# Optimization experiments

Hardware: AMD Instinct MI355X
Metric: run time of the kernel (lower is better)

The kernel has to match this reference:

```python
import jax, jax.numpy as jnp
import numpy as np

B, T, C = 32, 128, 64
E, H = 8, 4            # feat_dim, num_heads
D = E // H             # head_dim = 2
HID = 32               # hidden_dim


def setup_inputs() -> dict:
    key = jax.random.key(0)
    ks = jax.random.split(key, 20)
    s = 0.1
    return {
        "x": jax.random.normal(ks[0], (B, T, C), jnp.float32),
        # input_proj: Linear(C, C)
        "W_in": jax.random.normal(ks[1], (C, C), jnp.float32) * s,
        "b_in": jax.random.normal(ks[2], (C,), jnp.float32) * s,
        # time_step_score: Linear(C, C//4) -> GELU -> Linear(C//4, 1) -> Sigmoid
        "W_ts1": jax.random.normal(ks[3], (C // 4, C), jnp.float32) * s,
        "b_ts1": jax.random.normal(ks[4], (C // 4,), jnp.float32) * s,
        "W_ts2": jax.random.normal(ks[5], (1, C // 4), jnp.float32) * s,
        "b_ts2": jax.random.normal(ks[6], (1,), jnp.float32) * s,
        # per-channel GRU(1 -> E): torch gate order (r, z, n)
        "W_ih": jax.random.normal(ks[7], (C, 3 * E), jnp.float32) * s,      # input size 1
        "W_hh": jax.random.normal(ks[8], (C, 3 * E, E), jnp.float32) * s,
        "b_ih": jax.random.normal(ks[9], (C, 3 * E), jnp.float32) * s,
        "b_hh": jax.random.normal(ks[10], (C, 3 * E), jnp.float32) * s,
        # shared MultiheadAttention(E, 4): packed in_proj + out_proj
        "W_qkv": jax.random.normal(ks[11], (3 * E, E), jnp.float32) * s,
        "b_qkv": jax.random.normal(ks[12], (3 * E,), jnp.float32) * s,
        "W_o": jax.random.normal(ks[13], (E, E), jnp.float32) * s,
        "b_o": jax.random.normal(ks[14], (E,), jnp.float32) * s,
        # out_proj: Linear(C*E, HID)
        "W_out": jax.random.normal(ks[15], (HID, C * E), jnp.float32) * s,
        "b_out": jax.random.normal(ks[16], (HID,), jnp.float32) * s,
    }


def _forward(x, W_in, b_in, W_ts1, b_ts1, W_ts2, b_ts2,
             W_ih, W_hh, b_ih, b_hh, W_qkv, b_qkv, W_o, b_o, W_out, b_out):
    bs, ts, c = x.shape
    # time step importance: per-timestep MLP over the raw features
    h1 = jax.nn.gelu(jnp.einsum('btc,fc->btf', x, W_ts1) + b_ts1, approximate=False)
    ts_imp = jax.nn.sigmoid(jnp.einsum('btf,of->bto', h1, W_ts2) + b_ts2)[..., 0]  # [B,T]

    xp = jnp.einsum('btc,dc->btd', x, W_in) + b_in  # [B,T,C]

    # Batched per-channel GRU scan over time. state h: [B,C,E]
    def step(h, x_t):
        gi = x_t[:, :, None] * W_ih[None] + b_ih          # [B,C,3E]
        gh = jnp.einsum('bce,cge->bcg', h, W_hh) + b_hh   # [B,C,3E]
        ir, iz, inn = gi[..., :E], gi[..., E:2 * E], gi[..., 2 * E:]
        hr, hz, hn = gh[..., :E], gh[..., E:2 * E], gh[..., 2 * E:]
        r = jax.nn.sigmoid(ir + hr)
        z = jax.nn.sigmoid(iz + hz)
        n = jnp.tanh(inn + r * hn)
        h_new = (1.0 - z) * n + z * h
        return h_new, h_new

    h0 = jnp.zeros((bs, c, E), xp.dtype)
    _, hs = jax.lax.scan(step, h0, jnp.transpose(xp, (1, 0, 2)))  # [T,B,C,E]
    hs_bcte = jnp.transpose(hs, (1, 2, 0, 3))                     # [B,C,T,E]

    # Shared MHA applied independently per channel (batched over B*C)
    qkv = jnp.einsum('bcte,fe->bctf', hs_bcte, W_qkv) + b_qkv     # [B,C,T,3E]
    q, k, v = qkv[..., :E], qkv[..., E:2 * E], qkv[..., 2 * E:]
    def heads(t):
        return t.reshape(bs, c, ts, H, D)
    q, k, v = heads(q), heads(k), heads(v)
    scores = jnp.einsum('bcthd,bcshd->bchts', q, k) / np.sqrt(D)
    attn = jax.nn.softmax(scores, axis=-1)
    o = jnp.einsum('bchts,bcshd->bcthd', attn, v).reshape(bs, c, ts, E)
    attn_out = jnp.einsum('bcte,fe->bctf', o, W_o) + b_o          # [B,C,T,E]
    attention = jnp.transpose(attn_out, (0, 2, 1, 3))             # [B,T,C,E]

    out_flat = jnp.transpose(hs, (1, 0, 2, 3)).reshape(bs, ts, c * E)  # [B,T,C*E]
    out = jnp.einsum('btf,hf->bth', out_flat, W_out) + b_out           # [B,T,HID]

    feat_imp = jax.nn.sigmoid(attention.sum(axis=(1, 3)))   # [B,C]
    tsf_imp = jax.nn.sigmoid(attention.sum(axis=-1))        # [B,T,C]
    return out[:, -1, :], feat_imp, ts_imp, tsf_imp


def reference(x, W_in, b_in, W_ts1, b_ts1, W_ts2, b_ts2,
              W_ih, W_hh, b_ih, b_hh, W_qkv, b_qkv, W_o, b_o, W_out, b_out):
    return _forward(x, W_in, b_in, W_ts1, b_ts1, W_ts2, b_ts2,
                    W_ih, W_hh, b_ih, b_hh, W_qkv, b_qkv, W_o, b_o, W_out, b_out)
```

## Files before the change

kernel.cpp:

```cpp
#include <hip/hip_runtime.h>
#include <hip/hip_bf16.h>
#include <math.h>

#define B_ 32
#define T_ 128
#define C_ 64
#define E_ 8
#define HID_ 32

#define LOG2E 1.44269504088896341f

__device__ __forceinline__ float fast_rcp(float x) { return __builtin_amdgcn_rcpf(x); }
__device__ __forceinline__ float fast_sigmoid(float x) {
    return fast_rcp(1.0f + exp2f(-LOG2E * x));
}
__device__ __forceinline__ float fast_tanh(float x) {
    float xc = fminf(fmaxf(x, -15.0f), 15.0f);
    float t = exp2f(2.0f * LOG2E * xc);
    return (t - 1.0f) * fast_rcp(t + 1.0f);
}

__global__ __launch_bounds__(64) void k_gru(
    const float* __restrict__ x, const float* __restrict__ W_in, const float* __restrict__ b_in,
    const float* __restrict__ W_ih, const float* __restrict__ W_hh,
    const float* __restrict__ b_ih, const float* __restrict__ b_hh,
    float* __restrict__ hs, float* __restrict__ fh)
{
    const int tid = threadIdx.x;
    const int ci = tid >> 3;
    const int e = tid & 7;
    const int chain = blockIdx.x * 8 + ci;
    const int b = chain >> 6;
    const int c = chain & 63;

    __shared__ float wsh[8][C_];
    __shared__ float xc[8][T_ + 1];

#pragma unroll
    for (int i = 0; i < 8; ++i) {
        int idx = tid * 8 + i;
        int ci2 = idx >> 6;
        int cc = (blockIdx.x * 8 + ci2) & 63;
        wsh[ci2][idx & 63] = W_in[cc * C_ + (idx & 63)];
    }
    __syncthreads();

    const float bi = b_in[c];
    for (int tt = 0; tt < 16; ++tt) {
        const int t = e * 16 + tt;
        const float4* xr = (const float4*)(x + (b * T_ + t) * C_);
        float a = bi;
#pragma unroll
        for (int k4 = 0; k4 < 16; ++k4) {
            float4 xv = xr[k4];
            a = fmaf(xv.x, wsh[ci][k4 * 4 + 0], a);
            a = fmaf(xv.y, wsh[ci][k4 * 4 + 1], a);
            a = fmaf(xv.z, wsh[ci][k4 * 4 + 2], a);
            a = fmaf(xv.w, wsh[ci][k4 * 4 + 3], a);
        }
        xc[ci][t] = a;
    }
    __syncthreads();

    float wr[E_], wz[E_], wn[E_];
#pragma unroll
    for (int j = 0; j < E_; ++j) {
        wr[j] = W_hh[(c * 24 + 0 * E_ + e) * E_ + j];
        wz[j] = W_hh[(c * 24 + 1 * E_ + e) * E_ + j];
        wn[j] = W_hh[(c * 24 + 2 * E_ + e) * E_ + j];
    }
    const float wir = W_ih[c * 24 + e], wiz = W_ih[c * 24 + E_ + e], win = W_ih[c * 24 + 2 * E_ + e];
    const float bir = b_ih[c * 24 + e], biz = b_ih[c * 24 + E_ + e], bin_ = b_ih[c * 24 + 2 * E_ + e];
    const float bhr = b_hh[c * 24 + e], bhz = b_hh[c * 24 + E_ + e], bhn = b_hh[c * 24 + 2 * E_ + e];

    float h = 0.0f;
    float* ho = hs + (size_t)chain * T_ * E_ + e;
    for (int t = 0; t < T_; ++t) {
        float xv = xc[ci][t];
        float gr = fmaf(xv, wir, bir) + bhr;
        float gz = fmaf(xv, wiz, biz) + bhz;
        float gn = fmaf(xv, win, bin_);
        float hn = bhn;
#pragma unroll
        for (int j = 0; j < E_; ++j) {
            float hj = __shfl(h, j, E_);
            gr = fmaf(hj, wr[j], gr);
            gz = fmaf(hj, wz[j], gz);
            hn = fmaf(hj, wn[j], hn);
        }
        float r = fast_sigmoid(gr);
        float z = fast_sigmoid(gz);
        float nn = fast_tanh(fmaf(r, hn, gn));
        h = fmaf(z, h - nn, nn);
        ho[t * E_] = h;
    }
    fh[chain * E_ + e] = h;
}

__global__ __launch_bounds__(128) void k_attn(
    const float* __restrict__ hs, const float* __restrict__ W_qkv, const float* __restrict__ b_qkv,
    const float* __restrict__ W_o, const float* __restrict__ b_o,
    float* __restrict__ feat_imp, float* __restrict__ tsf_imp)
{
    const int bc = blockIdx.x;
    const int b = bc >> 6, c = bc & 63;
    const int tid = threadIdx.x;
    const int r = tid >> 1;
    const int p = tid & 1;

    __shared__ __align__(16) float hsl[T_][E_];
    __shared__ __align__(16) float ks[T_][E_];
    __shared__ __align__(16) float vs[T_][E_];
    __shared__ float wssum[E_];
    __shared__ float bsum_s;
    __shared__ float red[T_];

    {
        const float4* hp = (const float4*)(hs + (size_t)bc * T_ * E_ + tid * E_);
        ((float4*)&hsl[tid][0])[0] = hp[0];
        ((float4*)&hsl[tid][0])[1] = hp[1];
    }
    if (tid < E_) {
        float ws = 0.0f;
#pragma unroll
        for (int fp = 0; fp < E_; ++fp) ws += W_o[fp * E_ + tid];
        wssum[tid] = ws;
    }
    if (tid == E_) {
        float bs = 0.0f;
#pragma unroll
        for (int fp = 0; fp < E_; ++fp) bs += b_o[fp];
        bsum_s = bs;
    }
    __syncthreads();

    const float qscale = 0.70710678118654752f * LOG2E;
    {
        float hr[E_];
#pragma unroll
        for (int j = 0; j < E_; ++j) hr[j] = hsl[tid][j];
#pragma unroll
        for (int f = 0; f < E_; ++f) {
            float a = b_qkv[E_ + f];
#pragma unroll
            for (int j = 0; j < E_; ++j) a = fmaf(hr[j], W_qkv[(E_ + f) * E_ + j], a);
            ks[tid][f] = a;
        }
#pragma unroll
        for (int f = 0; f < E_; ++f) {
            float a = b_qkv[2 * E_ + f];
#pragma unroll
            for (int j = 0; j < E_; ++j) a = fmaf(hr[j], W_qkv[(2 * E_ + f) * E_ + j], a);
            vs[tid][f] = a;
        }
    }
    float q0[E_], q1[E_];
#pragma unroll
    for (int f = 0; f < E_; ++f) {
        float a0 = b_qkv[f], a1 = b_qkv[f];
#pragma unroll
        for (int j = 0; j < E_; ++j) {
            float w = W_qkv[f * E_ + j];
            a0 = fmaf(hsl[r][j], w, a0);
            a1 = fmaf(hsl[r + 64][j], w, a1);
        }
        q0[f] = a0 * qscale;
        q1[f] = a1 * qscale;
    }
    __syncthreads();

    float l0[4] = {0.f,0.f,0.f,0.f}, l1[4] = {0.f,0.f,0.f,0.f};
    float a0[E_] = {0.f,0.f,0.f,0.f,0.f,0.f,0.f,0.f};
    float a1[E_] = {0.f,0.f,0.f,0.f,0.f,0.f,0.f,0.f};
    const float* kb = &ks[p * 64][0];
    const float* vb = &vs[p * 64][0];
#pragma unroll 8
    for (int i = 0; i < 64; ++i) {
        float4 k0 = *(const float4*)(kb + i * 8);
        float4 k1 = *(const float4*)(kb + i * 8 + 4);
        float4 v0 = *(const float4*)(vb + i * 8);
        float4 v1 = *(const float4*)(vb + i * 8 + 4);
        float p00 = exp2f(fmaf(q0[1], k0.y, q0[0] * k0.x));
        float p01 = exp2f(fmaf(q0[3], k0.w, q0[2] * k0.z));
        float p02 = exp2f(fmaf(q0[5], k1.y, q0[4] * k1.x));
        float p03 = exp2f(fmaf(q0[7], k1.w, q0[6] * k1.z));
        float p10 = exp2f(fmaf(q1[1], k0.y, q1[0] * k0.x));
        float p11 = exp2f(fmaf(q1[3], k0.w, q1[2] * k0.z));
        float p12 = exp2f(fmaf(q1[5], k1.y, q1[4] * k1.x));
        float p13 = exp2f(fmaf(q1[7], k1.w, q1[6] * k1.z));
        l0[0] += p00; l0[1] += p01; l0[2] += p02; l0[3] += p03;
        l1[0] += p10; l1[1] += p11; l1[2] += p12; l1[3] += p13;
        a0[0] = fmaf(p00, v0.x, a0[0]); a0[1] = fmaf(p00, v0.y, a0[1]);
        a0[2] = fmaf(p01, v0.z, a0[2]); a0[3] = fmaf(p01, v0.w, a0[3]);
        a0[4] = fmaf(p02, v1.x, a0[4]); a0[5] = fmaf(p02, v1.y, a0[5]);
        a0[6] = fmaf(p03, v1.z, a0[6]); a0[7] = fmaf(p03, v1.w, a0[7]);
        a1[0] = fmaf(p10, v0.x, a1[0]); a1[1] = fmaf(p10, v0.y, a1[1]);
        a1[2] = fmaf(p11, v0.z, a1[2]); a1[3] = fmaf(p11, v0.w, a1[3]);
        a1[4] = fmaf(p12, v1.x, a1[4]); a1[5] = fmaf(p12, v1.y, a1[5]);
        a1[6] = fmaf(p13, v1.z, a1[6]); a1[7] = fmaf(p13, v1.w, a1[7]);
    }

#pragma unroll
    for (int i = 0; i < 4; ++i) {
        l0[i] += __shfl_xor(l0[i], 1);
        l1[i] += __shfl_xor(l1[i], 1);
    }
#pragma unroll
    for (int j = 0; j < E_; ++j) {
        a0[j] += __shfl_xor(a0[j], 1);
        a1[j] += __shfl_xor(a1[j], 1);
    }

    const float* lm = p ? l1 : l0;
    const float* am = p ? a1 : a0;
    const int row = p ? (r + 64) : r;
    float S = bsum_s;
#pragma unroll
    for (int f = 0; f < E_; ++f)
        S = fmaf(am[f] * fast_rcp(lm[f >> 1]), wssum[f], S);

    tsf_imp[(size_t)b * T_ * C_ + (size_t)row * C_ + c] = fast_sigmoid(S);
    red[row] = S;
    __syncthreads();
    for (int off = 64; off > 0; off >>= 1) {
        if (tid < off) red[tid] += red[tid + off];
        __syncthreads();
    }
    if (tid == 0) feat_imp[bc] = fast_sigmoid(red[0]);
}

__global__ __launch_bounds__(64) void k_ts(
    const float* __restrict__ x,
    const float* __restrict__ W_ts1, const float* __restrict__ b_ts1,
    const float* __restrict__ W_ts2, const float* __restrict__ b_ts2,
    float* __restrict__ ts_imp)
{
    const int bt = blockIdx.x;
    const int tid = threadIdx.x;
    __shared__ float xs[C_];
    __shared__ float h1[16];
    xs[tid] = x[bt * C_ + tid];
    __syncthreads();
    if (tid < 16) {
        float a = b_ts1[tid];
#pragma unroll
        for (int k = 0; k < C_; ++k) a = fmaf(xs[k], W_ts1[tid * C_ + k], a);
        h1[tid] = 0.5f * a * (1.0f + erff(a * 0.70710678118654752f));
    }
    __syncthreads();
    if (tid == 0) {
        float s = b_ts2[0];
#pragma unroll
        for (int k = 0; k < 16; ++k) s = fmaf(h1[k], W_ts2[k], s);
        ts_imp[bt] = fast_sigmoid(s);
    }
}

__global__ __launch_bounds__(64) void k_out(
    const float* __restrict__ fh, const float* __restrict__ W_out, const float* __restrict__ b_out,
    float* __restrict__ out0)
{
    const int b = blockIdx.x;
    const int tid = threadIdx.x;
    __shared__ float hf[C_ * E_];
    const float4* src = (const float4*)(fh + (b * C_ + tid) * E_);
    float4* dst = (float4*)(hf + tid * E_);
    dst[0] = src[0];
    dst[1] = src[1];
    __syncthreads();
    if (tid < HID_) {
        float a = b_out[tid];
        const float* wo = W_out + tid * (C_ * E_);
        for (int k = 0; k < C_ * E_; ++k) a = fmaf(hf[k], wo[k], a);
        out0[b * HID_ + tid] = a;
    }
}

extern "C" void kernel_launch(void* const* d_in, const int* in_sizes, int n_in,
                              void* d_out, int out_size, void* d_ws, size_t ws_size,
                              hipStream_t stream) {
    (void)in_sizes; (void)n_in; (void)out_size; (void)ws_size;

    float* out0 = (float*)d_out;
    float* feat = out0 + B_ * HID_;
    float* tsim = feat + B_ * C_;
    float* tsf  = tsim + B_ * T_;

    const float* x     = (const float*)d_in[0];
    const float* W_in  = (const float*)d_in[1];
    const float* b_in  = (const float*)d_in[2];
    const float* W_ts1 = (const float*)d_in[3];
    const float* b_ts1 = (const float*)d_in[4];
    const float* W_ts2 = (const float*)d_in[5];
    const float* b_ts2 = (const float*)d_in[6];
    const float* W_ih  = (const float*)d_in[7];
    const float* W_hh  = (const float*)d_in[8];
    const float* b_ih  = (const float*)d_in[9];
    const float* b_hh  = (const float*)d_in[10];
    const float* W_qkv = (const float*)d_in[11];
    const float* b_qkv = (const float*)d_in[12];
    const float* W_o   = (const float*)d_in[13];
    const float* b_o   = (const float*)d_in[14];
    const float* W_out = (const float*)d_in[15];
    const float* b_out = (const float*)d_in[16];

    float* fhb = (float*)d_ws;
    float* hsb = fhb + B_ * C_ * E_;

    hipLaunchKernelGGL(k_gru, dim3(B_ * C_ / 8), dim3(64), 0, stream,
                       x, W_in, b_in, W_ih, W_hh, b_ih, b_hh, hsb, fhb);
    hipLaunchKernelGGL(k_attn, dim3(B_ * C_), dim3(128), 0, stream,
                       hsb, W_qkv, b_qkv, W_o, b_o, feat, tsf);
    hipLaunchKernelGGL(k_ts, dim3(B_ * T_), dim3(64), 0, stream,
                       x, W_ts1, b_ts1, W_ts2, b_ts2, tsim);
    hipLaunchKernelGGL(k_out, dim3(B_), dim3(64), 0, stream,
                       fhb, W_out, b_out, out0);
}
```

Before: 110.6 us.

## Fold W_o into V, split attention keys across 256 threads, shorten GRU dependency chain

The attention kernel now only computes what the outputs need: the sum over output features. It precomputes per-row dot products of V with the column sums of W_o, so it no longer accumulates the full 8-wide P·V. Keys are split across four 64-thread groups (256 threads per block), and the partial softmax sums are combined through shared memory. In the GRU recurrence, the matvec is rewritten as a tree of pairwise products instead of a serial FMA chain, the r/z biases are pre-added and the next input is prefetched, all to cut per-step latency. This adds extra shared memory and a synchronization step for the partial reduction, and the x prefetch reads one element past the end of each row on the last step.

```diff
diff --git a/kernel.cpp b/kernel.cpp
--- a/kernel.cpp
+++ b/kernel.cpp
@@ -15,7 +15,7 @@
     return fast_rcp(1.0f + exp2f(-LOG2E * x));
 }
 __device__ __forceinline__ float fast_tanh(float x) {
-    float xc = fminf(fmaxf(x, -15.0f), 15.0f);
+    float xc = __builtin_amdgcn_fmed3f(x, -15.0f, 15.0f);
     float t = exp2f(2.0f * LOG2E * xc);
     return (t - 1.0f) * fast_rcp(t + 1.0f);
 }
@@ -70,34 +70,49 @@
         wn[j] = W_hh[(c * 24 + 2 * E_ + e) * E_ + j];
     }
     const float wir = W_ih[c * 24 + e], wiz = W_ih[c * 24 + E_ + e], win = W_ih[c * 24 + 2 * E_ + e];
-    const float bir = b_ih[c * 24 + e], biz = b_ih[c * 24 + E_ + e], bin_ = b_ih[c * 24 + 2 * E_ + e];
-    const float bhr = b_hh[c * 24 + e], bhz = b_hh[c * 24 + E_ + e], bhn = b_hh[c * 24 + 2 * E_ + e];
+    const float cr = b_ih[c * 24 + e] + b_hh[c * 24 + e];
+    const float cz = b_ih[c * 24 + E_ + e] + b_hh[c * 24 + E_ + e];
+    const float bin_ = b_ih[c * 24 + 2 * E_ + e];
+    const float bhn  = b_hh[c * 24 + 2 * E_ + e];
 
     float h = 0.0f;
+    float xv = xc[ci][0];
     float* ho = hs + (size_t)chain * T_ * E_ + e;
     for (int t = 0; t < T_; ++t) {
-        float xv = xc[ci][t];
-        float gr = fmaf(xv, wir, bir) + bhr;
-        float gz = fmaf(xv, wiz, biz) + bhz;
-        float gn = fmaf(xv, win, bin_);
-        float hn = bhn;
-#pragma unroll
-        for (int j = 0; j < E_; ++j) {
-            float hj = __shfl(h, j, E_);
-            gr = fmaf(hj, wr[j], gr);
-            gz = fmaf(hj, wz[j], gz);
-            hn = fmaf(hj, wn[j], hn);
-        }
+        float xvn = xc[ci][t + 1];
+        float hj0 = __shfl(h, 0, 8), hj1 = __shfl(h, 1, 8);
+        float hj2 = __shfl(h, 2, 8), hj3 = __shfl(h, 3, 8);
+        float hj4 = __shfl(h, 4, 8), hj5 = __shfl(h, 5, 8);
+        float hj6 = __shfl(h, 6, 8), hj7 = __shfl(h, 7, 8);
+        float grx = fmaf(xv, wir, cr);
+        float gzx = fmaf(xv, wiz, cz);
+        float gnx = fmaf(xv, win, bin_);
+        float r0 = fmaf(hj1, wr[1], hj0 * wr[0]);
+        float r1 = fmaf(hj3, wr[3], hj2 * wr[2]);
+        float r2 = fmaf(hj5, wr[5], hj4 * wr[4]);
+        float r3 = fmaf(hj7, wr[7], hj6 * wr[6]);
+        float z0 = fmaf(hj1, wz[1], hj0 * wz[0]);
+        float z1 = fmaf(hj3, wz[3], hj2 * wz[2]);
+        float z2 = fmaf(hj5, wz[5], hj4 * wz[4]);
+        float z3 = fmaf(hj7, wz[7], hj6 * wz[6]);
+        float n0 = fmaf(hj1, wn[1], hj0 * wn[0]);
+        float n1 = fmaf(hj3, wn[3], hj2 * wn[2]);
+        float n2 = fmaf(hj5, wn[5], hj4 * wn[4]);
+        float n3 = fmaf(hj7, wn[7], hj6 * wn[6]);
+        float gr = grx + ((r0 + r1) + (r2 + r3));
+        float gz = gzx + ((z0 + z1) + (z2 + z3));
+        float hn = bhn + ((n0 + n1) + (n2 + n3));
         float r = fast_sigmoid(gr);
         float z = fast_sigmoid(gz);
-        float nn = fast_tanh(fmaf(r, hn, gn));
+        float nn = fast_tanh(fmaf(r, hn, gnx));
         h = fmaf(z, h - nn, nn);
         ho[t * E_] = h;
+        xv = xvn;
     }
     fh[chain * E_ + e] = h;
 }
 
-__global__ __launch_bounds__(128) void k_attn(
+__global__ __launch_bounds__(256) void k_attn(
     const float* __restrict__ hs, const float* __restrict__ W_qkv, const float* __restrict__ b_qkv,
     const float* __restrict__ W_o, const float* __restrict__ b_o,
     float* __restrict__ feat_imp, float* __restrict__ tsf_imp)
@@ -105,81 +120,80 @@
     const int bc = blockIdx.x;
     const int b = bc >> 6, c = bc & 63;
     const int tid = threadIdx.x;
-    const int r = tid >> 1;
-    const int p = tid & 1;
-
-    __shared__ __align__(16) float hsl[T_][E_];
+    const int t2 = tid & 63;
+    const int sq = tid >> 6;
+
     __shared__ __align__(16) float ks[T_][E_];
-    __shared__ __align__(16) float vs[T_][E_];
-    __shared__ float wssum[E_];
-    __shared__ float bsum_s;
+    __shared__ __align__(16) float us[T_][4];
+    __shared__ float qsT[E_][T_];
+    __shared__ float pacc[3][T_][8];
     __shared__ float red[T_];
 
+    const float qscale = 0.70710678118654752f * LOG2E;
+
     {
-        const float4* hp = (const float4*)(hs + (size_t)bc * T_ * E_ + tid * E_);
-        ((float4*)&hsl[tid][0])[0] = hp[0];
-        ((float4*)&hsl[tid][0])[1] = hp[1];
-    }
-    if (tid < E_) {
-        float ws = 0.0f;
-#pragma unroll
-        for (int fp = 0; fp < E_; ++fp) ws += W_o[fp * E_ + tid];
-        wssum[tid] = ws;
-    }
-    if (tid == E_) {
-        float bs = 0.0f;
-#pragma unroll
-        for (int fp = 0; fp < E_; ++fp) bs += b_o[fp];
-        bsum_s = bs;
-    }
-    __syncthreads();
-
-    const float qscale = 0.70710678118654752f * LOG2E;
-    {
-        float hr[E_];
-#pragma unroll
-        for (int j = 0; j < E_; ++j) hr[j] = hsl[tid][j];
-#pragma unroll
-        for (int f = 0; f < E_; ++f) {
-            float a = b_qkv[E_ + f];
-#pragma unroll
-            for (int j = 0; j < E_; ++j) a = fmaf(hr[j], W_qkv[(E_ + f) * E_ + j], a);
-            ks[tid][f] = a;
+        const int row = (tid < 128) ? tid : (tid - 128);
+        const float4* hp = (const float4*)(hs + (size_t)bc * T_ * E_ + row * E_);
+        float4 h0 = hp[0], h1 = hp[1];
+        float hr[E_] = {h0.x, h0.y, h0.z, h0.w, h1.x, h1.y, h1.z, h1.w};
+        if (tid < 128) {
+            float kv[E_];
+#pragma unroll
+            for (int f = 0; f < E_; ++f) {
+                float a = b_qkv[E_ + f];
+#pragma unroll
+                for (int j = 0; j < E_; ++j) a = fmaf(hr[j], W_qkv[(E_ + f) * E_ + j], a);
+                kv[f] = a;
+            }
+            ((float4*)&ks[row][0])[0] = make_float4(kv[0], kv[1], kv[2], kv[3]);
+            ((float4*)&ks[row][0])[1] = make_float4(kv[4], kv[5], kv[6], kv[7]);
+#pragma unroll
+            for (int f = 0; f < E_; ++f) {
+                float a = b_qkv[f];
+#pragma unroll
+                for (int j = 0; j < E_; ++j) a = fmaf(hr[j], W_qkv[f * E_ + j], a);
+                qsT[f][row] = a * qscale;
+            }
+        } else {
+            float ws[E_];
+#pragma unroll
+            for (int d = 0; d < E_; ++d) {
+                float w = 0.0f;
+#pragma unroll
+                for (int fp = 0; fp < E_; ++fp) w += W_o[fp * E_ + d];
+                ws[d] = w;
+            }
+            float vv[E_];
+#pragma unroll
+            for (int f = 0; f < E_; ++f) {
+                float a = b_qkv[2 * E_ + f];
+#pragma unroll
+                for (int j = 0; j < E_; ++j) a = fmaf(hr[j], W_qkv[(2 * E_ + f) * E_ + j], a);
+                vv[f] = a;
+            }
+            float4 uu;
+            uu.x = fmaf(vv[1], ws[1], vv[0] * ws[0]);
+            uu.y = fmaf(vv[3], ws[3], vv[2] * ws[2]);
+            uu.z = fmaf(vv[5], ws[5], vv[4] * ws[4]);
+            uu.w = fmaf(vv[7], ws[7], vv[6] * ws[6]);
+            *((float4*)&us[row][0]) = uu;
         }
-#pragma unroll
-        for (int f = 0; f < E_; ++f) {
-            float a = b_qkv[2 * E_ + f];
-#pragma unroll
-            for (int j = 0; j < E_; ++j) a = fmaf(hr[j], W_qkv[(2 * E_ + f) * E_ + j], a);
-            vs[tid][f] = a;
-        }
-    }
+    }
+    __syncthreads();
+
     float q0[E_], q1[E_];
 #pragma unroll
-    for (int f = 0; f < E_; ++f) {
-        float a0 = b_qkv[f], a1 = b_qkv[f];
-#pragma unroll
-        for (int j = 0; j < E_; ++j) {
-            float w = W_qkv[f * E_ + j];
-            a0 = fmaf(hsl[r][j], w, a0);
-            a1 = fmaf(hsl[r + 64][j], w, a1);
-        }
-        q0[f] = a0 * qscale;
-        q1[f] = a1 * qscale;
-    }
-    __syncthreads();
-
-    float l0[4] = {0.f,0.f,0.f,0.f}, l1[4] = {0.f,0.f,0.f,0.f};
-    float a0[E_] = {0.f,0.f,0.f,0.f,0.f,0.f,0.f,0.f};
-    float a1[E_] = {0.f,0.f,0.f,0.f,0.f,0.f,0.f,0.f};
-    const float* kb = &ks[p * 64][0];
-    const float* vb = &vs[p * 64][0];
+    for (int f = 0; f < E_; ++f) { q0[f] = qsT[f][t2]; q1[f] = qsT[f][t2 + 64]; }
+
+    float l0[4] = {0.f,0.f,0.f,0.f}, S0[4] = {0.f,0.f,0.f,0.f};
+    float l1[4] = {0.f,0.f,0.f,0.f}, S1[4] = {0.f,0.f,0.f,0.f};
+    const float* kb = &ks[sq * 32][0];
+    const float* ub = &us[sq * 32][0];
 #pragma unroll 8
-    for (int i = 0; i < 64; ++i) {
+    for (int i = 0; i < 32; ++i) {
         float4 k0 = *(const float4*)(kb + i * 8);
         float4 k1 = *(const float4*)(kb + i * 8 + 4);
-        float4 v0 = *(const float4*)(vb + i * 8);
-        float4 v1 = *(const float4*)(vb + i * 8 + 4);
+        float4 uu = *(const float4*)(ub + i * 4);
         float p00 = exp2f(fmaf(q0[1], k0.y, q0[0] * k0.x));
         float p01 = exp2f(fmaf(q0[3], k0.w, q0[2] * k0.z));
         float p02 = exp2f(fmaf(q0[5], k1.y, q0[4] * k1.x));
@@ -190,37 +204,45 @@
         float p13 = exp2f(fmaf(q1[7], k1.w, q1[6] * k1.z));
         l0[0] += p00; l0[1] += p01; l0[2] += p02; l0[3] += p03;
         l1[0] += p10; l1[1] += p11; l1[2] += p12; l1[3] += p13;
-        a0[0] = fmaf(p00, v0.x, a0[0]); a0[1] = fmaf(p00, v0.y, a0[1]);
-        a0[2] = fmaf(p01, v0.z, a0[2]); a0[3] = fmaf(p01, v0.w, a0[3]);
-        a0[4] = fmaf(p02, v1.x, a0[4]); a0[5] = fmaf(p02, v1.y, a0[5]);
-        a0[6] = fmaf(p03, v1.z, a0[6]); a0[7] = fmaf(p03, v1.w, a0[7]);
-        a1[0] = fmaf(p10, v0.x, a1[0]); a1[1] = fmaf(p10, v0.y, a1[1]);
-        a1[2] = fmaf(p11, v0.z, a1[2]); a1[3] = fmaf(p11, v0.w, a1[3]);
-        a1[4] = fmaf(p12, v1.x, a1[4]); a1[5] = fmaf(p12, v1.y, a1[5]);
-        a1[6] = fmaf(p13, v1.z, a1[6]); a1[7] = fmaf(p13, v1.w, a1[7]);
-    }
-
-#pragma unroll
-    for (int i = 0; i < 4; ++i) {
-        l0[i] += __shfl_xor(l0[i], 1);
-        l1[i] += __shfl_xor(l1[i], 1);
-    }
-#pragma unroll
-    for (int j = 0; j < E_; ++j) {
-        a0[j] += __shfl_xor(a0[j], 1);
-        a1[j] += __shfl_xor(a1[j], 1);
-    }
-
-    const float* lm = p ? l1 : l0;
-    const float* am = p ? a1 : a0;
-    const int row = p ? (r + 64) : r;
-    float S = bsum_s;
-#pragma unroll
-    for (int f = 0; f < E_; ++f)
-        S = fmaf(am[f] * fast_rcp(lm[f >> 1]), wssum[f], S);
-
-    tsf_imp[(size_t)b * T_ * C_ + (size_t)row * C_ + c] = fast_sigmoid(S);
-    red[row] = S;
+        S0[0] = fmaf(p00, uu.x, S0[0]); S0[1] = fmaf(p01, uu.y, S0[1]);
+        S0[2] = fmaf(p02, uu.z, S0[2]); S0[3] = fmaf(p03, uu.w, S0[3]);
+        S1[0] = fmaf(p10, uu.x, S1[0]); S1[1] = fmaf(p11, uu.y, S1[1]);
+        S1[2] = fmaf(p12, uu.z, S1[2]); S1[3] = fmaf(p13, uu.w, S1[3]);
+    }
+
+    if (sq > 0) {
+        float* pr = &pacc[sq - 1][t2][0];
+#pragma unroll
+        for (int i = 0; i < 4; ++i) { pr[i] = l0[i]; pr[4 + i] = S0[i]; }
+        pr = &pacc[sq - 1][t2 + 64][0];
+#pragma unroll
+        for (int i = 0; i < 4; ++i) { pr[i] = l1[i]; pr[4 + i] = S1[i]; }
+    }
+    __syncthreads();
+
+    if (sq == 0) {
+        float bsum = 0.0f;
+#pragma unroll
+        for (int fp = 0; fp < E_; ++fp) bsum += b_o[fp];
+#pragma unroll
+        for (int qq = 0; qq < 3; ++qq) {
+#pragma unroll
+            for (int i = 0; i < 4; ++i) {
+                l0[i] += pacc[qq][t2][i];       S0[i] += pacc[qq][t2][4 + i];
+                l1[i] += pacc[qq][t2 + 64][i];  S1[i] += pacc[qq][t2 + 64][4 + i];
+            }
+        }
+        float Sa = bsum, Sb = bsum;
+#pragma unroll
+        for (int hh = 0; hh < 4; ++hh) {
+            Sa = fmaf(S0[hh], fast_rcp(l0[hh]), Sa);
+            Sb = fmaf(S1[hh], fast_rcp(l1[hh]), Sb);
+        }
+        tsf_imp[(size_t)b * T_ * C_ + (size_t)t2 * C_ + c] = fast_sigmoid(Sa);
+        tsf_imp[(size_t)b * T_ * C_ + (size_t)(t2 + 64) * C_ + c] = fast_sigmoid(Sb);
+        red[t2] = Sa;
+        red[t2 + 64] = Sb;
+    }
     __syncthreads();
     for (int off = 64; off > 0; off >>= 1) {
         if (tid < off) red[tid] += red[tid + off];
@@ -309,7 +331,7 @@
 
     hipLaunchKernelGGL(k_gru, dim3(B_ * C_ / 8), dim3(64), 0, stream,
                        x, W_in, b_in, W_ih, W_hh, b_ih, b_hh, hsb, fhb);
-    hipLaunchKernelGGL(k_attn, dim3(B_ * C_), dim3(128), 0, stream,
+    hipLaunchKernelGGL(k_attn, dim3(B_ * C_), dim3(256), 0, stream,
                        hsb, W_qkv, b_qkv, W_o, b_o, feat, tsf);
     hipLaunchKernelGGL(k_ts, dim3(B_ * T_), dim3(64), 0, stream,
                        x, W_ts1, b_ts1, W_ts2, b_ts2, tsim);
```

After: 93.19 us. -15.7%, faster.
